# Kernel tuning notes

Hardware: AMD Instinct MI355X
Metric: run time of the kernel (lower is better)

The kernel has to match this reference:

```python
import jax, jax.numpy as jnp
import numpy as np

D_MODEL = 1024
D_STATE = 16
D_CONV = 4
EXPAND = 2
D_INNER = D_MODEL * EXPAND          # 2048
DT_RANK = max(D_MODEL // 16, 1)     # 64
BATCH, SEQ_LEN = 2, 1024


def setup_inputs() -> dict:
    key = jax.random.key(0)
    ks = jax.random.split(key, 10)
    s = 0.02  # torch init std for linears
    x = jax.random.normal(ks[0], (BATCH, SEQ_LEN, D_MODEL), jnp.float32)
    W_in = jax.random.normal(ks[1], (2 * D_INNER, D_MODEL), jnp.float32) * s
    conv_w = jax.random.normal(ks[2], (D_INNER, 1, D_CONV), jnp.float32) * (1.0 / np.sqrt(D_CONV))
    conv_b = jnp.zeros((D_INNER,), jnp.float32)
    W_x = jax.random.normal(ks[3], (DT_RANK + 2 * D_STATE, D_INNER), jnp.float32) * s
    W_dt = jax.random.uniform(ks[4], (D_INNER, DT_RANK), jnp.float32,
                              -DT_RANK ** -0.5, DT_RANK ** -0.5)
    # dt bias init: inverse-softplus of dt ~ LogUniform(1e-3, 1e-1)
    dt = jnp.exp(jax.random.uniform(ks[5], (D_INNER,), jnp.float32)
                 * (np.log(0.1) - np.log(0.001)) + np.log(0.001))
    b_dt = dt + jnp.log(-jnp.expm1(-dt))
    A_log = jnp.log(jnp.tile(jnp.arange(1, D_STATE + 1, dtype=jnp.float32), (D_INNER, 1)))
    D_skip = jnp.ones((D_INNER,), jnp.float32)
    W_out = jax.random.normal(ks[6], (D_MODEL, D_INNER), jnp.float32) * s
    return {"x": x, "W_in": W_in, "conv_w": conv_w, "conv_b": conv_b, "W_x": W_x,
            "W_dt": W_dt, "b_dt": b_dt, "A_log": A_log, "D_skip": D_skip, "W_out": W_out}


def _causal_depthwise_conv(x_bld, conv_w, conv_b):
    # x_bld: [B, L, d_inner]; conv_w: [d_inner, 1, K]. Torch pads K-1 both
    # sides then slices [:seq_len] == causal left-pad of K-1.
    K = conv_w.shape[-1]
    lhs = jnp.pad(x_bld, ((0, 0), (K - 1, 0), (0, 0))).transpose(0, 2, 1)  # [B, C, L+K-1]
    out = jax.lax.conv_general_dilated(
        lhs, conv_w, window_strides=(1,), padding='VALID',
        dimension_numbers=('NCH', 'OIH', 'NCH'),
        feature_group_count=conv_w.shape[0])
    return out.transpose(0, 2, 1) + conv_b  # [B, L, d_inner]


def reference(x, W_in, conv_w, conv_b, W_x, W_dt, b_dt, A_log, D_skip, W_out):
    d_inner = W_in.shape[0] // 2
    dt_rank = W_dt.shape[1]
    d_state = A_log.shape[1]

    xz = jnp.einsum('bld,ed->ble', x, W_in)            # [B, L, 2*d_inner]
    x_ssm, z = xz[..., :d_inner], xz[..., d_inner:]
    x_ssm = jax.nn.silu(_causal_depthwise_conv(x_ssm, conv_w, conv_b))

    dbc = jnp.einsum('bld,ed->ble', x_ssm, W_x)        # [B, L, dt_rank+2*d_state]
    dt = jax.nn.softplus(jnp.einsum('blr,dr->bld', dbc[..., :dt_rank], W_dt) + b_dt)
    Bm = dbc[..., dt_rank:dt_rank + d_state]           # [B, L, d_state]
    Cm = dbc[..., dt_rank + d_state:]                  # [B, L, d_state]

    A = -jnp.exp(A_log)                                # [d_inner, d_state]
    A_bar = jnp.exp(dt[..., None] * A)                 # [B, L, d_inner, d_state]
    x_db = (x_ssm * dt)[..., None] * Bm[:, :, None, :] # [B, L, d_inner, d_state]

    def step(h, inp):
        a_t, xb_t, c_t = inp                           # [B,d,n], [B,d,n], [B,n]
        h = a_t * h + xb_t
        y_t = jnp.einsum('bn,bdn->bd', c_t, h)
        return h, y_t

    h0 = jnp.zeros((x.shape[0], d_inner, d_state), x.dtype)
    _, ys = jax.lax.scan(step, h0, (jnp.swapaxes(A_bar, 0, 1),
                                    jnp.swapaxes(x_db, 0, 1),
                                    jnp.swapaxes(Cm, 0, 1)))
    y = jnp.swapaxes(ys, 0, 1)                         # [B, L, d_inner]
    y = (y + x_ssm * D_skip) * jax.nn.silu(z)
    return jnp.einsum('bld,od->blo', y, W_out)         # [B, L, d_model]
```

## Files before the change

kernel.cpp:

```cpp
#include <hip/hip_runtime.h>
#include <hip/hip_bf16.h>
#include <math.h>

#define D_MODEL 1024
#define D_STATE 16
#define D_INNER 2048
#define DT_RANK 64
#define BATCH 2
#define SEQ_LEN 1024
#define T_TOTAL (BATCH * SEQ_LEN)

#define NC 16
#define CL 64

#define KS 16
#define KC 128
#define KT 64

typedef unsigned short u16;
typedef __bf16 bf16x8 __attribute__((ext_vector_type(8)));
typedef float f32x4 __attribute__((ext_vector_type(4)));

__device__ __forceinline__ u16 f2bf(float f) {
    unsigned u = __builtin_bit_cast(unsigned, f);
    u += 0x7FFFu + ((u >> 16) & 1u);
    return (u16)(u >> 16);
}

#define GLOAD_LDS16(g, l) \
    __builtin_amdgcn_global_load_lds((const __attribute__((address_space(1))) void*)(g), \
                                     (__attribute__((address_space(3))) void*)(l), 16, 0, 0)

__global__ __launch_bounds__(256) void cast_bf16_kernel(
    const float* __restrict__ in, u16* __restrict__ out)
{
    int i = blockIdx.x * 256 + threadIdx.x;
    float4 v = ((const float4*)in)[i];
    unsigned lo = (unsigned)f2bf(v.x) | ((unsigned)f2bf(v.y) << 16);
    unsigned hi = (unsigned)f2bf(v.z) | ((unsigned)f2bf(v.w) << 16);
    ((uint2*)out)[i] = make_uint2(lo, hi);
}

__global__ __launch_bounds__(256) void gemm_bf16_bt(
    const u16* __restrict__ A, int lda,
    const u16* __restrict__ Bw, int ldb,
    float* __restrict__ C, int ldc, int K)
{
    __shared__ u16 As[128][32];
    __shared__ u16 Bs[128][32];

    const int tid  = threadIdx.x;
    const int lane = tid & 63;
    const int wave = tid >> 6;
    const int wr   = wave >> 1;
    const int wc   = wave & 1;
    const int row0 = blockIdx.y * 128;
    const int col0 = blockIdx.x * 128;

    const int srow = tid >> 2;
    const int scol = (tid & 3) * 8;

    const u16* ag = A  + (size_t)(row0 + srow) * lda + scol;
    const u16* bg = Bw + (size_t)(col0 + srow) * ldb + scol;
    u16* asl = &As[0][0] + wave * 512;
    u16* bsl = &Bs[0][0] + wave * 512;

    f32x4 acc[4][4];
#pragma unroll
    for (int m = 0; m < 4; ++m)
#pragma unroll
        for (int n = 0; n < 4; ++n)
            acc[m][n] = (f32x4){0.f, 0.f, 0.f, 0.f};

    const int fr = lane & 15;
    const int kh = (lane >> 4) * 8;

    for (int k0 = 0; k0 < K; k0 += 32) {
        GLOAD_LDS16(ag + k0,                      asl);
        GLOAD_LDS16(ag + k0 + (size_t)64 * lda,   asl + 2048);
        GLOAD_LDS16(bg + k0,                      bsl);
        GLOAD_LDS16(bg + k0 + (size_t)64 * ldb,   bsl + 2048);
        __syncthreads();

        bf16x8 af[4], bf[4];
#pragma unroll
        for (int m = 0; m < 4; ++m)
            af[m] = *(const bf16x8*)&As[wr * 64 + m * 16 + fr][kh];
#pragma unroll
        for (int n = 0; n < 4; ++n)
            bf[n] = *(const bf16x8*)&Bs[wc * 64 + n * 16 + fr][kh];
#pragma unroll
        for (int m = 0; m < 4; ++m)
#pragma unroll
            for (int n = 0; n < 4; ++n)
                acc[m][n] = __builtin_amdgcn_mfma_f32_16x16x32_bf16(
                    af[m], bf[n], acc[m][n], 0, 0, 0);
        __syncthreads();
    }

    const int crow = (lane >> 4) * 4;
#pragma unroll
    for (int m = 0; m < 4; ++m) {
        const int gr = row0 + wr * 64 + m * 16 + crow;
#pragma unroll
        for (int n = 0; n < 4; ++n) {
            const int gc = col0 + wc * 64 + n * 16 + fr;
#pragma unroll
            for (int r = 0; r < 4; ++r)
                C[(size_t)(gr + r) * ldc + gc] = acc[m][n][r];
        }
    }
}

__global__ __launch_bounds__(256) void wx_partial(
    const float* __restrict__ A,
    const float* __restrict__ Bw,
    float* __restrict__ part)
{
    __shared__ float As[32][68];
    __shared__ float Bs[KT][98];

    const int tid = threadIdx.x;
    const int ks  = blockIdx.x;
    const int m0  = blockIdx.y * 32;
    const int k0  = ks * KC;

    const int tx = tid & 15;
    const int ty = tid >> 4;

    float acc[2][6] = {};

    for (int kk = 0; kk < KC; kk += KT) {
#pragma unroll
        for (int i = 0; i < 2; ++i) {
            int slot = tid + i * 256;
            int m  = slot >> 4;
            int kq = slot & 15;
            float4 v = *(const float4*)&A[(size_t)(m0 + m) * D_INNER + k0 + kk + kq * 4];
            *(float4*)&As[m][kq * 4] = v;
        }
#pragma unroll
        for (int i = 0; i < 6; ++i) {
            int slot = tid + i * 256;
            int n  = slot >> 4;
            int kq = slot & 15;
            float4 v = *(const float4*)&Bw[(size_t)n * D_INNER + k0 + kk + kq * 4];
            Bs[kq * 4 + 0][n] = v.x;
            Bs[kq * 4 + 1][n] = v.y;
            Bs[kq * 4 + 2][n] = v.z;
            Bs[kq * 4 + 3][n] = v.w;
        }
        __syncthreads();

#pragma unroll 8
        for (int k = 0; k < KT; ++k) {
            float a0 = As[ty * 2 + 0][k];
            float a1 = As[ty * 2 + 1][k];
            float2 b0 = *(const float2*)&Bs[k][tx * 6 + 0];
            float2 b1 = *(const float2*)&Bs[k][tx * 6 + 2];
            float2 b2 = *(const float2*)&Bs[k][tx * 6 + 4];
            float bv[6] = {b0.x, b0.y, b1.x, b1.y, b2.x, b2.y};
#pragma unroll
            for (int j = 0; j < 6; ++j) {
                acc[0][j] += a0 * bv[j];
                acc[1][j] += a1 * bv[j];
            }
        }
        __syncthreads();
    }

#pragma unroll
    for (int i = 0; i < 2; ++i) {
        size_t base = ((size_t)ks * T_TOTAL + (m0 + ty * 2 + i)) * 96 + tx * 6;
#pragma unroll
        for (int j = 0; j < 6; ++j)
            part[base + j] = acc[i][j];
    }
}

__global__ __launch_bounds__(256) void wx_reduce(
    const float* __restrict__ part, float* __restrict__ dbc)
{
    int i = blockIdx.x * 256 + threadIdx.x;
    float s = 0.f;
#pragma unroll
    for (int ks = 0; ks < KS; ++ks)
        s += part[(size_t)ks * T_TOTAL * 96 + i];
    dbc[i] = s;
}

__global__ __launch_bounds__(256) void dt_gemm(
    const float* __restrict__ A,
    const float* __restrict__ Bw,
    const float* __restrict__ bdt,
    float* __restrict__ dtb)
{
    __shared__ float As[16][65];
    __shared__ float Bs[16][65];

    const int tid = threadIdx.x;
    const int row0 = blockIdx.y * 64;
    const int col0 = blockIdx.x * 64;
    const int ty = tid >> 4;
    const int tx = tid & 15;

    float acc[4][4] = {};

    for (int k0 = 0; k0 < DT_RANK; k0 += 16) {
#pragma unroll
        for (int i = 0; i < 4; ++i) {
            int idx = tid + i * 256;
            int m = idx >> 4;
            int k = idx & 15;
            As[k][m] = A[(size_t)(row0 + m) * 96 + (k0 + k)];
        }
#pragma unroll
        for (int i = 0; i < 4; ++i) {
            int idx = tid + i * 256;
            int n = idx >> 4;
            int k = idx & 15;
            Bs[k][n] = Bw[(size_t)(col0 + n) * DT_RANK + (k0 + k)];
        }
        __syncthreads();

#pragma unroll
        for (int k = 0; k < 16; ++k) {
            float a[4], b[4];
#pragma unroll
            for (int i = 0; i < 4; ++i) a[i] = As[k][ty * 4 + i];
#pragma unroll
            for (int j = 0; j < 4; ++j) b[j] = Bs[k][tx * 4 + j];
#pragma unroll
            for (int i = 0; i < 4; ++i)
#pragma unroll
                for (int j = 0; j < 4; ++j)
                    acc[i][j] += a[i] * b[j];
        }
        __syncthreads();
    }

#pragma unroll
    for (int i = 0; i < 4; ++i) {
        int gm = row0 + ty * 4 + i;
#pragma unroll
        for (int j = 0; j < 4; ++j) {
            int gn = col0 + tx * 4 + j;
            float xv = acc[i][j] + bdt[gn];
            float sp = (xv > 20.f) ? xv : log1pf(__expf(xv));
            dtb[(size_t)gm * D_INNER + gn] = sp;
        }
    }
}

__global__ __launch_bounds__(256) void conv_silu_kernel(
    const float* __restrict__ xz,
    const float* __restrict__ cw,
    const float* __restrict__ cb,
    float* __restrict__ xc)
{
    int idx = blockIdx.x * 256 + threadIdx.x;
    int d = idx & (D_INNER - 1);
    int t = (idx >> 11) & (SEQ_LEN - 1);
    int b = idx >> 21;

    const float* base = xz + ((size_t)b * SEQ_LEN + t) * (2 * D_INNER) + d;
    float w0 = cw[d * 4 + 0], w1 = cw[d * 4 + 1], w2 = cw[d * 4 + 2], w3 = cw[d * 4 + 3];
    float acc = cb[d];
    if (t >= 3) acc += w0 * base[-3 * (2 * D_INNER)];
    if (t >= 2) acc += w1 * base[-2 * (2 * D_INNER)];
    if (t >= 1) acc += w2 * base[-1 * (2 * D_INNER)];
    acc += w3 * base[0];
    float s = acc / (1.f + __expf(-acc));
    xc[idx] = s;
}

__global__ __launch_bounds__(256) void scan_phaseA(
    const float* __restrict__ dbc,
    const float* __restrict__ dtv,
    const float* __restrict__ xc,
    const float* __restrict__ A_log,
    float* __restrict__ hf,
    float* __restrict__ Pf)
{
    __shared__ float sB[CL][16];
    __shared__ float sdt[CL][16];
    __shared__ float sx[CL][16];

    const int tid = threadIdx.x;
    const int n  = tid & 15;
    const int dl = tid >> 4;
    const int c  = blockIdx.x;
    const int d0 = blockIdx.y * 16;
    const int b  = blockIdx.z;
    const int t0 = c * CL;
    const int d  = d0 + dl;

#pragma unroll
    for (int i = 0; i < 4; ++i) {
        int f = tid + i * 256;
        int t = f >> 4;
        int e = f & 15;
        size_t row = (size_t)(b * SEQ_LEN + t0 + t);
        sB[t][e]  = dbc[row * 96 + DT_RANK + e];
        sdt[t][e] = dtv[row * D_INNER + d0 + e];
        sx[t][e]  = xc [row * D_INNER + d0 + e];
    }
    __syncthreads();

    const float A = -__expf(A_log[d * 16 + n]);

    float h = 0.f, p = 1.f;
#pragma unroll 4
    for (int t = 0; t < CL; ++t) {
        float dtval = sdt[t][dl];
        float a = __expf(dtval * A);
        h = a * h + (sx[t][dl] * dtval) * sB[t][n];
        p *= a;
    }
    size_t o = (((size_t)(b * NC + c) * D_INNER) + d) * 16 + n;
    hf[o] = h;
    Pf[o] = p;
}

__global__ __launch_bounds__(256) void scan_phaseB(
    const float* __restrict__ hf,
    const float* __restrict__ Pf,
    float* __restrict__ H0)
{
    int idx = blockIdx.x * 256 + threadIdx.x;
    int b  = idx >> 15;
    int dn = idx & 32767;
    float h = 0.f;
#pragma unroll
    for (int c = 0; c < NC; ++c) {
        size_t o = (((size_t)(b * NC + c)) << 15) + dn;
        H0[o] = h;
        h = Pf[o] * h + hf[o];
    }
}

__global__ __launch_bounds__(256) void scan_phaseC(
    const float* __restrict__ dbc,
    const float* __restrict__ dtv,
    const float* __restrict__ xc,
    const float* __restrict__ xz,
    const float* __restrict__ A_log,
    const float* __restrict__ D_skip,
    const float* __restrict__ H0,
    u16* __restrict__ y)
{
    __shared__ float sB[CL][16];
    __shared__ float sC[CL][16];
    __shared__ float sdt[CL][16];
    __shared__ float sx[CL][16];
    __shared__ float sz[CL][16];

    const int tid = threadIdx.x;
    const int n  = tid & 15;
    const int dl = tid >> 4;
    const int c  = blockIdx.x;
    const int d0 = blockIdx.y * 16;
    const int b  = blockIdx.z;
    const int t0 = c * CL;
    const int d  = d0 + dl;

#pragma unroll
    for (int i = 0; i < 4; ++i) {
        int f = tid + i * 256;
        int t = f >> 4;
        int e = f & 15;
        size_t row = (size_t)(b * SEQ_LEN + t0 + t);
        sB[t][e]  = dbc[row * 96 + DT_RANK + e];
        sC[t][e]  = dbc[row * 96 + DT_RANK + D_STATE + e];
        sdt[t][e] = dtv[row * D_INNER + d0 + e];
        sx[t][e]  = xc [row * D_INNER + d0 + e];
        sz[t][e]  = xz [row * (2 * D_INNER) + D_INNER + d0 + e];
    }
    __syncthreads();

    const float A  = -__expf(A_log[d * 16 + n]);
    const float Dv = D_skip[d];

    float h = H0[(((size_t)(b * NC + c) * D_INNER) + d) * 16 + n];
    u16* yb = y + (size_t)(b * SEQ_LEN + t0) * D_INNER + d;

#pragma unroll 4
    for (int t = 0; t < CL; ++t) {
        float dtval = sdt[t][dl];
        float xv = sx[t][dl];
        float a = __expf(dtval * A);
        h = a * h + (xv * dtval) * sB[t][n];
        float p = sC[t][n] * h;
        p += __shfl_xor(p, 1);
        p += __shfl_xor(p, 2);
        p += __shfl_xor(p, 4);
        p += __shfl_xor(p, 8);
        if (n == 0) {
            float zv = sz[t][dl];
            float sig = 1.f / (1.f + __expf(-zv));
            yb[(size_t)t * D_INNER] = f2bf((p + xv * Dv) * (zv * sig));
        }
    }
}

extern "C" void kernel_launch(void* const* d_in, const int* in_sizes, int n_in,
                              void* d_out, int out_size, void* d_ws, size_t ws_size,
                              hipStream_t stream)
{
    const float* x      = (const float*)d_in[0];
    const float* W_in   = (const float*)d_in[1];
    const float* conv_w = (const float*)d_in[2];
    const float* conv_b = (const float*)d_in[3];
    const float* W_x    = (const float*)d_in[4];
    const float* W_dt   = (const float*)d_in[5];
    const float* b_dt   = (const float*)d_in[6];
    const float* A_log  = (const float*)d_in[7];
    const float* D_skip = (const float*)d_in[8];
    const float* W_out  = (const float*)d_in[9];
    float* out = (float*)d_out;

    float* ws = (float*)d_ws;
    float* xz    = ws;
    float* xc    = xz + (size_t)8388608;
    float* dbc   = xc + (size_t)4194304;
    float* dtbuf = dbc + (size_t)196608;
    float* hf    = dtbuf + (size_t)4194304;
    float* Pf    = hf + (size_t)1048576;
    float* H0    = Pf + (size_t)1048576;
    u16* ybf = (u16*)(H0 + (size_t)1048576);
    u16* xbf = ybf + (size_t)4194304;
    u16* wbf = xbf + (size_t)2097152;
    float* part = dtbuf;

    cast_bf16_kernel<<<2048, 256, 0, stream>>>(x, xbf);
    cast_bf16_kernel<<<4096, 256, 0, stream>>>(W_in, wbf);

    {
        dim3 grid(4096 / 128, 2048 / 128);
        gemm_bf16_bt<<<grid, 256, 0, stream>>>(xbf, D_MODEL, wbf, D_MODEL,
                                               xz, 2 * D_INNER, D_MODEL);
    }
    conv_silu_kernel<<<(T_TOTAL * D_INNER) / 256, 256, 0, stream>>>(xz, conv_w, conv_b, xc);

    {
        dim3 grid(KS, T_TOTAL / 32);
        wx_partial<<<grid, 256, 0, stream>>>(xc, W_x, part);
        wx_reduce<<<(T_TOTAL * 96) / 256, 256, 0, stream>>>(part, dbc);
    }
    {
        dim3 grid(D_INNER / 64, T_TOTAL / 64);
        dt_gemm<<<grid, 256, 0, stream>>>(dbc, W_dt, b_dt, dtbuf);
    }
    {
        dim3 gridA(NC, D_INNER / 16, BATCH);
        scan_phaseA<<<gridA, 256, 0, stream>>>(dbc, dtbuf, xc, A_log, hf, Pf);
        scan_phaseB<<<(BATCH * D_INNER * 16) / 256, 256, 0, stream>>>(hf, Pf, H0);
        scan_phaseC<<<gridA, 256, 0, stream>>>(dbc, dtbuf, xc, xz,
                                               A_log, D_skip, H0, ybf);
    }
    cast_bf16_kernel<<<2048, 256, 0, stream>>>(W_out, wbf);

    {
        dim3 grid(1024 / 128, 2048 / 128);
        gemm_bf16_bt<<<grid, 256, 0, stream>>>(ybf, D_INNER, wbf, D_INNER,
                                               out, D_MODEL, D_INNER);
    }
}
```

Baseline: 334.4 us.

## Restructure chunked scan to one channel per thread with 16 register states

```diff
diff --git a/kernel.cpp b/kernel.cpp
--- a/kernel.cpp
+++ b/kernel.cpp
@@ -10,8 +10,8 @@
 #define SEQ_LEN 1024
 #define T_TOTAL (BATCH * SEQ_LEN)
 
-#define NC 16
-#define CL 64
+#define NC 64
+#define CL 16
 
 #define KS 16
 #define KC 128
@@ -274,132 +274,147 @@
     xc[idx] = s;
 }
 
-__global__ __launch_bounds__(256) void scan_phaseA(
+__global__ __launch_bounds__(256) void scanA(
     const float* __restrict__ dbc,
     const float* __restrict__ dtv,
     const float* __restrict__ xc,
     const float* __restrict__ A_log,
-    float* __restrict__ hf,
-    float* __restrict__ Pf)
+    float* __restrict__ hbuf,
+    float* __restrict__ sdt)
 {
     __shared__ float sB[CL][16];
-    __shared__ float sdt[CL][16];
-    __shared__ float sx[CL][16];
 
     const int tid = threadIdx.x;
-    const int n  = tid & 15;
-    const int dl = tid >> 4;
-    const int c  = blockIdx.x;
-    const int d0 = blockIdx.y * 16;
-    const int b  = blockIdx.z;
+    const int c = blockIdx.x;
+    const int b = blockIdx.z;
+    const int d = blockIdx.y * 256 + tid;
     const int t0 = c * CL;
-    const int d  = d0 + dl;
-
+
+    {
+        int t = tid >> 4, e = tid & 15;
+        sB[t][e] = dbc[(size_t)(b * SEQ_LEN + t0 + t) * 96 + DT_RANK + e];
+    }
+
+    float A[16];
 #pragma unroll
     for (int i = 0; i < 4; ++i) {
-        int f = tid + i * 256;
-        int t = f >> 4;
-        int e = f & 15;
-        size_t row = (size_t)(b * SEQ_LEN + t0 + t);
-        sB[t][e]  = dbc[row * 96 + DT_RANK + e];
-        sdt[t][e] = dtv[row * D_INNER + d0 + e];
-        sx[t][e]  = xc [row * D_INNER + d0 + e];
+        float4 v = *(const float4*)&A_log[d * 16 + i * 4];
+        A[i * 4 + 0] = -__expf(v.x);
+        A[i * 4 + 1] = -__expf(v.y);
+        A[i * 4 + 2] = -__expf(v.z);
+        A[i * 4 + 3] = -__expf(v.w);
     }
     __syncthreads();
 
-    const float A = -__expf(A_log[d * 16 + n]);
-
-    float h = 0.f, p = 1.f;
+    float h[16];
+#pragma unroll
+    for (int n = 0; n < 16; ++n) h[n] = 0.f;
+    float sum = 0.f;
+
 #pragma unroll 4
     for (int t = 0; t < CL; ++t) {
-        float dtval = sdt[t][dl];
-        float a = __expf(dtval * A);
-        h = a * h + (sx[t][dl] * dtval) * sB[t][n];
-        p *= a;
-    }
-    size_t o = (((size_t)(b * NC + c) * D_INNER) + d) * 16 + n;
-    hf[o] = h;
-    Pf[o] = p;
-}
-
-__global__ __launch_bounds__(256) void scan_phaseB(
-    const float* __restrict__ hf,
-    const float* __restrict__ Pf,
-    float* __restrict__ H0)
+        size_t row = (size_t)(b * SEQ_LEN + t0 + t);
+        float dtval = dtv[row * D_INNER + d];
+        float xv    = xc [row * D_INNER + d];
+        float w = xv * dtval;
+        sum += dtval;
+#pragma unroll
+        for (int n = 0; n < 16; ++n) {
+            float a = __expf(dtval * A[n]);
+            h[n] = a * h[n] + w * sB[t][n];
+        }
+    }
+
+    size_t o = (size_t)(b * NC + c) * 16 * D_INNER + d;
+#pragma unroll
+    for (int n = 0; n < 16; ++n)
+        hbuf[o + (size_t)n * D_INNER] = h[n];
+    sdt[(size_t)(b * NC + c) * D_INNER + d] = sum;
+}
+
+__global__ __launch_bounds__(256) void scanB(
+    const float* __restrict__ A_log,
+    const float* __restrict__ sdt,
+    float* __restrict__ hbuf)
 {
     int idx = blockIdx.x * 256 + threadIdx.x;
     int b  = idx >> 15;
-    int dn = idx & 32767;
+    int nd = idx & 32767;
+    int n  = nd >> 11;
+    int d  = nd & (D_INNER - 1);
+
+    const float A = -__expf(A_log[d * 16 + n]);
     float h = 0.f;
-#pragma unroll
+#pragma unroll 8
     for (int c = 0; c < NC; ++c) {
-        size_t o = (((size_t)(b * NC + c)) << 15) + dn;
-        H0[o] = h;
-        h = Pf[o] * h + hf[o];
-    }
-}
-
-__global__ __launch_bounds__(256) void scan_phaseC(
+        size_t o = ((size_t)(b * NC + c) * 16 + n) * D_INNER + d;
+        float tmp = hbuf[o];
+        float P = __expf(A * sdt[(size_t)(b * NC + c) * D_INNER + d]);
+        hbuf[o] = h;
+        h = P * h + tmp;
+    }
+}
+
+__global__ __launch_bounds__(256) void scanC(
     const float* __restrict__ dbc,
     const float* __restrict__ dtv,
     const float* __restrict__ xc,
     const float* __restrict__ xz,
     const float* __restrict__ A_log,
     const float* __restrict__ D_skip,
-    const float* __restrict__ H0,
+    const float* __restrict__ hbuf,
     u16* __restrict__ y)
 {
     __shared__ float sB[CL][16];
     __shared__ float sC[CL][16];
-    __shared__ float sdt[CL][16];
-    __shared__ float sx[CL][16];
-    __shared__ float sz[CL][16];
 
     const int tid = threadIdx.x;
-    const int n  = tid & 15;
-    const int dl = tid >> 4;
-    const int c  = blockIdx.x;
-    const int d0 = blockIdx.y * 16;
-    const int b  = blockIdx.z;
+    const int c = blockIdx.x;
+    const int b = blockIdx.z;
+    const int d = blockIdx.y * 256 + tid;
     const int t0 = c * CL;
-    const int d  = d0 + dl;
-
+
+    {
+        int t = tid >> 4, e = tid & 15;
+        size_t row = (size_t)(b * SEQ_LEN + t0 + t);
+        sB[t][e] = dbc[row * 96 + DT_RANK + e];
+        sC[t][e] = dbc[row * 96 + DT_RANK + D_STATE + e];
+    }
+
+    float A[16];
 #pragma unroll
     for (int i = 0; i < 4; ++i) {
-        int f = tid + i * 256;
-        int t = f >> 4;
-        int e = f & 15;
-        size_t row = (size_t)(b * SEQ_LEN + t0 + t);
-        sB[t][e]  = dbc[row * 96 + DT_RANK + e];
-        sC[t][e]  = dbc[row * 96 + DT_RANK + D_STATE + e];
-        sdt[t][e] = dtv[row * D_INNER + d0 + e];
-        sx[t][e]  = xc [row * D_INNER + d0 + e];
-        sz[t][e]  = xz [row * (2 * D_INNER) + D_INNER + d0 + e];
-    }
+        float4 v = *(const float4*)&A_log[d * 16 + i * 4];
+        A[i * 4 + 0] = -__expf(v.x);
+        A[i * 4 + 1] = -__expf(v.y);
+        A[i * 4 + 2] = -__expf(v.z);
+        A[i * 4 + 3] = -__expf(v.w);
+    }
+    const float Dv = D_skip[d];
+
+    float h[16];
+    size_t ho = (size_t)(b * NC + c) * 16 * D_INNER + d;
+#pragma unroll
+    for (int n = 0; n < 16; ++n)
+        h[n] = hbuf[ho + (size_t)n * D_INNER];
     __syncthreads();
-
-    const float A  = -__expf(A_log[d * 16 + n]);
-    const float Dv = D_skip[d];
-
-    float h = H0[(((size_t)(b * NC + c) * D_INNER) + d) * 16 + n];
-    u16* yb = y + (size_t)(b * SEQ_LEN + t0) * D_INNER + d;
 
 #pragma unroll 4
     for (int t = 0; t < CL; ++t) {
-        float dtval = sdt[t][dl];
-        float xv = sx[t][dl];
-        float a = __expf(dtval * A);
-        h = a * h + (xv * dtval) * sB[t][n];
-        float p = sC[t][n] * h;
-        p += __shfl_xor(p, 1);
-        p += __shfl_xor(p, 2);
-        p += __shfl_xor(p, 4);
-        p += __shfl_xor(p, 8);
-        if (n == 0) {
-            float zv = sz[t][dl];
-            float sig = 1.f / (1.f + __expf(-zv));
-            yb[(size_t)t * D_INNER] = f2bf((p + xv * Dv) * (zv * sig));
-        }
+        size_t row = (size_t)(b * SEQ_LEN + t0 + t);
+        float dtval = dtv[row * D_INNER + d];
+        float xv    = xc [row * D_INNER + d];
+        float zv    = xz [row * (2 * D_INNER) + D_INNER + d];
+        float w = xv * dtval;
+        float yv = 0.f;
+#pragma unroll
+        for (int n = 0; n < 16; ++n) {
+            float a = __expf(dtval * A[n]);
+            h[n] = a * h[n] + w * sB[t][n];
+            yv += sC[t][n] * h[n];
+        }
+        float sig = 1.f / (1.f + __expf(-zv));
+        y[row * D_INNER + d] = f2bf((yv + xv * Dv) * (zv * sig));
     }
 }
 
@@ -424,10 +439,9 @@
     float* xc    = xz + (size_t)8388608;
     float* dbc   = xc + (size_t)4194304;
     float* dtbuf = dbc + (size_t)196608;
-    float* hf    = dtbuf + (size_t)4194304;
-    float* Pf    = hf + (size_t)1048576;
-    float* H0    = Pf + (size_t)1048576;
-    u16* ybf = (u16*)(H0 + (size_t)1048576);
+    float* hbuf  = dtbuf + (size_t)4194304;
+    float* sdt   = hbuf + (size_t)4194304;
+    u16* ybf = (u16*)(sdt + (size_t)262144);
     u16* xbf = ybf + (size_t)4194304;
     u16* wbf = xbf + (size_t)2097152;
     float* part = dtbuf;
@@ -452,11 +466,11 @@
         dt_gemm<<<grid, 256, 0, stream>>>(dbc, W_dt, b_dt, dtbuf);
     }
     {
-        dim3 gridA(NC, D_INNER / 16, BATCH);
-        scan_phaseA<<<gridA, 256, 0, stream>>>(dbc, dtbuf, xc, A_log, hf, Pf);
-        scan_phaseB<<<(BATCH * D_INNER * 16) / 256, 256, 0, stream>>>(hf, Pf, H0);
-        scan_phaseC<<<gridA, 256, 0, stream>>>(dbc, dtbuf, xc, xz,
-                                               A_log, D_skip, H0, ybf);
+        dim3 gridA(NC, D_INNER / 256, BATCH);
+        scanA<<<gridA, 256, 0, stream>>>(dbc, dtbuf, xc, A_log, hbuf, sdt);
+        scanB<<<(BATCH * D_STATE * D_INNER) / 256, 256, 0, stream>>>(A_log, sdt, hbuf);
+        scanC<<<gridA, 256, 0, stream>>>(dbc, dtbuf, xc, xz,
+                                         A_log, D_skip, hbuf, ybf);
     }
     cast_bf16_kernel<<<2048, 256, 0, stream>>>(W_out, wbf);
 
```

After: 290.9 us. -13.0%, faster.
